# Kernel optimization log

Measured on AMD Instinct MI355X. Metric: run time of the kernel, lower is better.

The kernel has to match this reference:

```python
import jax, jax.numpy as jnp
import numpy as np

DIM = 1024
HEADS = 16
HEAD_DIM = DIM // HEADS
B, N = 4, 4096


def setup_inputs() -> dict:
    key = jax.random.key(0)
    k1, k2, k3, k4, k5 = jax.random.split(key, 5)
    scale_in = 1.0 / np.sqrt(DIM)
    return {
        "x": jax.random.normal(k1, (B, N, DIM), dtype=jnp.float32),
        # torch nn.Linear convention: weight [out, in], y = x @ W.T + b
        "w_qkv": jax.random.uniform(k2, (3 * DIM, DIM), jnp.float32, -scale_in, scale_in),
        "b_qkv": jax.random.uniform(k3, (3 * DIM,), jnp.float32, -scale_in, scale_in),
        "w_proj": jax.random.uniform(k4, (DIM, DIM), jnp.float32, -scale_in, scale_in),
        "b_proj": jax.random.uniform(k5, (DIM,), jnp.float32, -scale_in, scale_in),
    }


def reference(x, w_qkv, b_qkv, w_proj, b_proj):
    Bx, Nx, C = x.shape
    H, D = HEADS, HEAD_DIM
    qkv = (x @ w_qkv.T + b_qkv).reshape(Bx, Nx, 3, H, D)
    q, k, v = qkv[:, :, 0], qkv[:, :, 1], qkv[:, :, 2]  # each [B, N, H, D]
    # NOTE: faithful to source — heads dim was NOT moved to batch position,
    # so attention mixes across heads per token: scores [B, N, H, H].
    scores = jnp.einsum('bnhd,bngd->bnhg', q, k) / jnp.sqrt(jnp.asarray(D, x.dtype))
    attn = jax.nn.softmax(scores, axis=-1)
    out = jnp.einsum('bnhg,bngd->bnhd', attn, v).reshape(Bx, Nx, C)
    return out @ w_proj.T + b_proj
```

## Files before the change

### kernel.cpp

```cpp
#include <hip/hip_runtime.h>
#include <hip/hip_bf16.h>
#include <stdint.h>

typedef __bf16 v8bf __attribute__((ext_vector_type(8)));
typedef float  v4f  __attribute__((ext_vector_type(4)));
typedef unsigned short u16;

#define NTOK 16384
#define KDIM 1024

__device__ __forceinline__ u16 f2bf(float f) {
  uint32_t b = __builtin_bit_cast(uint32_t, f);
  b += 0x7FFFu + ((b >> 16) & 1u);
  return (u16)(b >> 16);
}

__device__ __forceinline__ void gl_lds16(const u16* g, u16* l) {
  __builtin_amdgcn_global_load_lds(
      (const __attribute__((address_space(1))) uint32_t*)g,
      (__attribute__((address_space(3))) uint32_t*)l,
      16, 0, 0);
}

__device__ __forceinline__ void bar() {
  __builtin_amdgcn_sched_barrier(0);
  __builtin_amdgcn_s_barrier();
  __builtin_amdgcn_sched_barrier(0);
}
#define LGKM0() do { asm volatile("s_waitcnt lgkmcnt(0)" ::: "memory"); \
                     __builtin_amdgcn_sched_barrier(0); } while (0)
#define VMW(n)  do { asm volatile("s_waitcnt vmcnt(" #n ")" ::: "memory"); \
                     __builtin_amdgcn_sched_barrier(0); } while (0)

__global__ void cvt_all(const float* __restrict__ x, const float* __restrict__ wq,
                        const float* __restrict__ wp, u16* __restrict__ xo,
                        u16* __restrict__ wqo, u16* __restrict__ wpo) {
  size_t id = (size_t)blockIdx.x * 256 + threadIdx.x;
  const float* src; u16* dst;
  if (id < 2097152)      { src = x  + id * 8;              dst = xo  + id * 8; }
  else if (id < 2490368) { src = wq + (id - 2097152) * 8;  dst = wqo + (id - 2097152) * 8; }
  else                   { src = wp + (id - 2490368) * 8;  dst = wpo + (id - 2490368) * 8; }
  float4 a = *(const float4*)(src);
  float4 b = *(const float4*)(src + 4);
  union { u16 u[8]; uint4 v; } pk;
  pk.u[0]=f2bf(a.x); pk.u[1]=f2bf(a.y); pk.u[2]=f2bf(a.z); pk.u[3]=f2bf(a.w);
  pk.u[4]=f2bf(b.x); pk.u[5]=f2bf(b.y); pk.u[6]=f2bf(b.z); pk.u[7]=f2bf(b.w);
  *(uint4*)(dst) = pk.v;
}

template<int NTOT, bool OUT_BF16>
__global__ __launch_bounds__(512, 1)
void gemm_bt(const u16* __restrict__ A, const u16* __restrict__ Bw,
             const float* __restrict__ bias, void* __restrict__ out) {
  constexpr int NM = NTOK / 256;
  constexpr int NN = NTOT / 256;
  constexpr int NWG = NM * NN;
  constexpr int NT = KDIM / 32;
  const int bid = blockIdx.x;
  const int swz = (bid & 7) * (NWG / 8) + (bid >> 3);
  const int bm = swz % NM, bn = swz / NM;

  extern __shared__ __align__(16) u16 smem[];
  u16* ldsA = smem;
  u16* ldsB = smem + 4 * 8192;

  const int tid = threadIdx.x, lane = tid & 63, w = tid >> 6;
  const int wr = w >> 2, wc = w & 3;

  v4f acc[8][4];
#pragma unroll
  for (int i = 0; i < 8; ++i)
#pragma unroll
    for (int j = 0; j < 4; ++j) acc[i][j] = v4f{0.f, 0.f, 0.f, 0.f};

  const u16* Ab = A  + (size_t)bm * 256 * KDIM;
  const u16* Bb = Bw + (size_t)bn * 256 * KDIM;

  const size_t soff0 = (size_t)(tid >> 2) * KDIM
      + (size_t)((((tid & 3) ^ ((tid >> 2) & 3) ^ ((tid >> 4) & 3)) & 3) * 8);
  auto stageT = [&](u16* dst, const u16* src) {
    gl_lds16(src + soff0, dst + (size_t)tid * 8);
    gl_lds16(src + soff0 + (size_t)128 * KDIM, dst + (size_t)tid * 8 + 4096);
  };

  const int cks = ((lane >> 4) ^ (lane & 3) ^ ((lane >> 2) & 3)) & 3;
  const int aoff = (wr * 128 + (lane & 15)) * 32 + cks * 8;
  const int boff = (wc * 64  + (lane & 15)) * 32 + cks * 8;

#define TILE(ST, U, DO_STAGE, VMODE) do {                                     \
  const u16* La_ = ldsA + (ST) * 8192;                                        \
  const u16* Lb_ = ldsB + (ST) * 8192;                                        \
  v8bf af[4], bf4[4];                                                         \
  _Pragma("unroll") for (int f = 0; f < 4; ++f)                               \
    af[f] = *(const v8bf*)(La_ + aoff + f * 512);                             \
  _Pragma("unroll") for (int f = 0; f < 4; ++f)                               \
    bf4[f] = *(const v8bf*)(Lb_ + boff + f * 512);                            \
  if (DO_STAGE) stageT(ldsA + (((ST) + 3) & 3) * 8192,                        \
                       Ab + (size_t)(U) * 32);                                \
  bar(); LGKM0();                                                             \
  __builtin_amdgcn_s_setprio(1);                                              \
  _Pragma("unroll") for (int qi = 0; qi < 4; ++qi)                            \
  _Pragma("unroll") for (int qj = 0; qj < 4; ++qj)                            \
    acc[qi][qj] = __builtin_amdgcn_mfma_f32_16x16x32_bf16(                    \
        af[qi], bf4[qj], acc[qi][qj], 0, 0, 0);                               \
  __builtin_amdgcn_s_setprio(0);                                              \
  bar();                                                                      \
  _Pragma("unroll") for (int f = 0; f < 4; ++f)                               \
    af[f] = *(const v8bf*)(La_ + aoff + (f + 4) * 512);                       \
  if (DO_STAGE) stageT(ldsB + (((ST) + 3) & 3) * 8192,                        \
                       Bb + (size_t)(U) * 32);                                \
  bar(); LGKM0();                                                             \
  __builtin_amdgcn_s_setprio(1);                                              \
  _Pragma("unroll") for (int qi = 0; qi < 4; ++qi)                            \
  _Pragma("unroll") for (int qj = 0; qj < 4; ++qj)                            \
    acc[4 + qi][qj] = __builtin_amdgcn_mfma_f32_16x16x32_bf16(                \
        af[qi], bf4[qj], acc[4 + qi][qj], 0, 0, 0);                           \
  __builtin_amdgcn_s_setprio(0);                                              \
  if ((VMODE) == 0) { VMW(8); }                                               \
  else if ((VMODE) == 1) { VMW(4); }                                          \
  else if ((VMODE) == 2) { VMW(0); }                                          \
  bar();                                                                      \
} while (0)

  stageT(ldsA + 0,     Ab);        stageT(ldsB + 0,     Bb);
  stageT(ldsA + 8192,  Ab + 32);   stageT(ldsB + 8192,  Bb + 32);
  stageT(ldsA + 16384, Ab + 64);   stageT(ldsB + 16384, Bb + 64);
  VMW(8);
  bar();

  for (int j = 0; j < 7; ++j) {
    const int t0 = 4 * j;
    TILE(0, t0 + 3, 1, 0);
    TILE(1, t0 + 4, 1, 0);
    TILE(2, t0 + 5, 1, 0);
    TILE(3, t0 + 6, 1, 0);
  }
  TILE(0, 31, 1, 0);
  TILE(1, 0, 0, 1);
  TILE(2, 0, 0, 2);
  TILE(3, 0, 0, 3);
#undef TILE

  const int col0 = bn * 256 + wc * 64 + (lane & 15);
  const int row0 = bm * 256 + wr * 128 + ((lane >> 4) << 2);
#pragma unroll
  for (int mf = 0; mf < 8; ++mf) {
#pragma unroll
    for (int nf = 0; nf < 4; ++nf) {
      const int gc = col0 + nf * 16;
      const float bv = bias[gc];
#pragma unroll
      for (int j = 0; j < 4; ++j) {
        const size_t idx = (size_t)(row0 + mf * 16 + j) * NTOT + gc;
        const float v = acc[mf][nf][j] + bv;
        if constexpr (OUT_BF16) ((u16*)out)[idx] = f2bf(v);
        else                    ((float*)out)[idx] = v;
      }
    }
  }
}

__global__ __launch_bounds__(256)
void attn_mix(const u16* __restrict__ qkv, u16* __restrict__ outp) {
  __shared__ __align__(16) u16 sq[4][3072];
  __shared__ float sp[4][16][16];
  const int tid = threadIdx.x, lane = tid & 63, w = tid >> 6;
  const size_t tok = (size_t)blockIdx.x * 4 + w;
  const u16* src = qkv + tok * 3072;
#pragma unroll
  for (int i = 0; i < 6; ++i) {
    int t = i * 64 + lane;
    int row = t >> 3;
    int c = (t & 7) ^ (row & 7);
    gl_lds16(src + row * 64 + c * 8, &sq[w][t * 8]);
  }
  __syncthreads();

  const int h = lane >> 2, gb = lane & 3;
  v8bf qv[8];
#pragma unroll
  for (int c = 0; c < 8; ++c)
    qv[c] = *(const v8bf*)&sq[w][h * 64 + ((c ^ (h & 7)) * 8)];

  float s[4];
#pragma unroll
  for (int g4 = 0; g4 < 4; ++g4) {
    const int g = gb * 4 + g4;
    float a = 0.f;
#pragma unroll
    for (int c = 0; c < 8; ++c) {
      v8bf kv = *(const v8bf*)&sq[w][1024 + g * 64 + ((c ^ (g & 7)) * 8)];
#pragma unroll
      for (int j = 0; j < 8; ++j) a += (float)qv[c][j] * (float)kv[j];
    }
    s[g4] = a * 0.125f;
  }
  float m = fmaxf(fmaxf(s[0], s[1]), fmaxf(s[2], s[3]));
  m = fmaxf(m, __shfl_xor(m, 1));
  m = fmaxf(m, __shfl_xor(m, 2));
  float p[4], sum = 0.f;
#pragma unroll
  for (int g4 = 0; g4 < 4; ++g4) { p[g4] = __expf(s[g4] - m); sum += p[g4]; }
  sum += __shfl_xor(sum, 1);
  sum += __shfl_xor(sum, 2);
  const float inv = 1.f / sum;
#pragma unroll
  for (int g4 = 0; g4 < 4; ++g4) sp[w][h][gb * 4 + g4] = p[g4] * inv;
  __syncthreads();

  float o[16];
#pragma unroll
  for (int j = 0; j < 16; ++j) o[j] = 0.f;
  const int db = gb;
#pragma unroll
  for (int g = 0; g < 16; ++g) {
    const float a = sp[w][h][g];
    v8bf v0 = *(const v8bf*)&sq[w][2048 + g * 64 + (((db * 2)     ^ (g & 7)) * 8)];
    v8bf v1 = *(const v8bf*)&sq[w][2048 + g * 64 + (((db * 2 + 1) ^ (g & 7)) * 8)];
#pragma unroll
    for (int j = 0; j < 8; ++j) { o[j] += a * (float)v0[j]; o[8 + j] += a * (float)v1[j]; }
  }
  union { u16 u[16]; uint4 v[2]; } ob;
#pragma unroll
  for (int j = 0; j < 16; ++j) ob.u[j] = f2bf(o[j]);
  u16* dst = outp + tok * 1024 + h * 64 + db * 16;
  *(uint4*)dst = ob.v[0];
  *((uint4*)dst + 1) = ob.v[1];
}

extern "C" void kernel_launch(void* const* d_in, const int* in_sizes, int n_in,
                              void* d_out, int out_size, void* d_ws, size_t ws_size,
                              hipStream_t stream) {
  const float* x      = (const float*)d_in[0];
  const float* w_qkv  = (const float*)d_in[1];
  const float* b_qkv  = (const float*)d_in[2];
  const float* w_proj = (const float*)d_in[3];
  const float* b_proj = (const float*)d_in[4];

  char* ws = (char*)d_ws;
  u16* x_bf    = (u16*)(ws);
  u16* wqkv_bf = (u16*)(ws + (size_t)33554432);
  u16* wp_bf   = (u16*)(ws + (size_t)39845888);
  u16* qkv_bf  = (u16*)(ws + (size_t)41943040);
  u16* at_bf   = (u16*)(ws + (size_t)142606336);

  (void)hipFuncSetAttribute((const void*)&gemm_bt<3072, true>,
                            hipFuncAttributeMaxDynamicSharedMemorySize, 131072);
  (void)hipFuncSetAttribute((const void*)&gemm_bt<1024, false>,
                            hipFuncAttributeMaxDynamicSharedMemorySize, 131072);

  cvt_all<<<dim3(10240), dim3(256), 0, stream>>>(x, w_qkv, w_proj,
                                                 x_bf, wqkv_bf, wp_bf);

  gemm_bt<3072, true ><<<dim3(768), dim3(512), 131072, stream>>>(x_bf, wqkv_bf, b_qkv, qkv_bf);
  attn_mix<<<dim3(4096), dim3(256), 0, stream>>>(qkv_bf, at_bf);
  gemm_bt<1024, false><<<dim3(256), dim3(512), 131072, stream>>>(at_bf, wp_bf, b_proj, d_out);
}
```

Baseline: 228.1 us.

## Double-buffer MFMA fragments in registers with one barrier per K-tile

After: 221.5 us. 2.9% less time.

```diff
diff --git a/kernel.cpp b/kernel.cpp
--- a/kernel.cpp
+++ b/kernel.cpp
@@ -49,7 +49,7 @@
 }
 
 template<int NTOT, bool OUT_BF16>
-__global__ __launch_bounds__(512, 1)
+__global__ __launch_bounds__(512, 2)
 void gemm_bt(const u16* __restrict__ A, const u16* __restrict__ Bw,
              const float* __restrict__ bias, void* __restrict__ out) {
   constexpr int NM = NTOK / 256;
@@ -87,39 +87,41 @@
   const int aoff = (wr * 128 + (lane & 15)) * 32 + cks * 8;
   const int boff = (wc * 64  + (lane & 15)) * 32 + cks * 8;
 
-#define TILE(ST, U, DO_STAGE, VMODE) do {                                     \
-  const u16* La_ = ldsA + (ST) * 8192;                                        \
-  const u16* Lb_ = ldsB + (ST) * 8192;                                        \
-  v8bf af[4], bf4[4];                                                         \
+  v8bf a0[4], b0[4], a1[4], b1[4];
+
+#define TILE(T, FA, FB, GA, GB, DOSTAGE, VMODE, DONEXT) do {                  \
+  const u16* La_c = ldsA + ((T) & 3) * 8192;                                  \
+  const u16* La_n = ldsA + (((T) + 1) & 3) * 8192;                            \
+  const u16* Lb_n = ldsB + (((T) + 1) & 3) * 8192;                            \
+  if ((VMODE) == 0) { VMW(4); } else if ((VMODE) == 1) { VMW(0); }            \
+  bar();                                                                      \
+  v8bf ab[4];                                                                 \
   _Pragma("unroll") for (int f = 0; f < 4; ++f)                               \
-    af[f] = *(const v8bf*)(La_ + aoff + f * 512);                             \
-  _Pragma("unroll") for (int f = 0; f < 4; ++f)                               \
-    bf4[f] = *(const v8bf*)(Lb_ + boff + f * 512);                            \
-  if (DO_STAGE) stageT(ldsA + (((ST) + 3) & 3) * 8192,                        \
-                       Ab + (size_t)(U) * 32);                                \
-  bar(); LGKM0();                                                             \
+    ab[f] = *(const v8bf*)(La_c + aoff + (f + 4) * 512);                      \
+  if (DOSTAGE) {                                                              \
+    stageT(ldsA + (((T) + 3) & 3) * 8192, Ab + (size_t)((T) + 3) * 32);       \
+    stageT(ldsB + (((T) + 3) & 3) * 8192, Bb + (size_t)((T) + 3) * 32);       \
+  }                                                                           \
   __builtin_amdgcn_s_setprio(1);                                              \
   _Pragma("unroll") for (int qi = 0; qi < 4; ++qi)                            \
   _Pragma("unroll") for (int qj = 0; qj < 4; ++qj)                            \
     acc[qi][qj] = __builtin_amdgcn_mfma_f32_16x16x32_bf16(                    \
-        af[qi], bf4[qj], acc[qi][qj], 0, 0, 0);                               \
+        FA[qi], FB[qj], acc[qi][qj], 0, 0, 0);                                \
   __builtin_amdgcn_s_setprio(0);                                              \
-  bar();                                                                      \
-  _Pragma("unroll") for (int f = 0; f < 4; ++f)                               \
-    af[f] = *(const v8bf*)(La_ + aoff + (f + 4) * 512);                       \
-  if (DO_STAGE) stageT(ldsB + (((ST) + 3) & 3) * 8192,                        \
-                       Bb + (size_t)(U) * 32);                                \
-  bar(); LGKM0();                                                             \
+  LGKM0();                                                                    \
+  if (DONEXT) {                                                               \
+    _Pragma("unroll") for (int f = 0; f < 4; ++f)                             \
+      GA[f] = *(const v8bf*)(La_n + aoff + f * 512);                          \
+    _Pragma("unroll") for (int f = 0; f < 4; ++f)                             \
+      GB[f] = *(const v8bf*)(Lb_n + boff + f * 512);                          \
+  }                                                                           \
   __builtin_amdgcn_s_setprio(1);                                              \
   _Pragma("unroll") for (int qi = 0; qi < 4; ++qi)                            \
   _Pragma("unroll") for (int qj = 0; qj < 4; ++qj)                            \
     acc[4 + qi][qj] = __builtin_amdgcn_mfma_f32_16x16x32_bf16(                \
-        af[qi], bf4[qj], acc[4 + qi][qj], 0, 0, 0);                           \
+        ab[qi], FB[qj], acc[4 + qi][qj], 0, 0, 0);                            \
   __builtin_amdgcn_s_setprio(0);                                              \
-  if ((VMODE) == 0) { VMW(8); }                                               \
-  else if ((VMODE) == 1) { VMW(4); }                                          \
-  else if ((VMODE) == 2) { VMW(0); }                                          \
-  bar();                                                                      \
+  LGKM0();                                                                    \
 } while (0)
 
   stageT(ldsA + 0,     Ab);        stageT(ldsB + 0,     Bb);
@@ -127,18 +129,21 @@
   stageT(ldsA + 16384, Ab + 64);   stageT(ldsB + 16384, Bb + 64);
   VMW(8);
   bar();
-
-  for (int j = 0; j < 7; ++j) {
-    const int t0 = 4 * j;
-    TILE(0, t0 + 3, 1, 0);
-    TILE(1, t0 + 4, 1, 0);
-    TILE(2, t0 + 5, 1, 0);
-    TILE(3, t0 + 6, 1, 0);
-  }
-  TILE(0, 31, 1, 0);
-  TILE(1, 0, 0, 1);
-  TILE(2, 0, 0, 2);
-  TILE(3, 0, 0, 3);
+#pragma unroll
+  for (int f = 0; f < 4; ++f) a0[f] = *(const v8bf*)(ldsA + aoff + f * 512);
+#pragma unroll
+  for (int f = 0; f < 4; ++f) b0[f] = *(const v8bf*)(ldsB + boff + f * 512);
+  LGKM0();
+
+  for (int j = 0; j < 14; ++j) {
+    const int t0 = 2 * j;
+    TILE(t0,     a0, b0, a1, b1, 1, 0, 1);
+    TILE(t0 + 1, a1, b1, a0, b0, 1, 0, 1);
+  }
+  TILE(28, a0, b0, a1, b1, 1, 0, 1);
+  TILE(29, a1, b1, a0, b0, 0, 0, 1);
+  TILE(30, a0, b0, a1, b1, 0, 1, 1);
+  TILE(31, a1, b1, a0, b0, 0, 2, 0);
 #undef TILE
 
   const int col0 = bn * 256 + wc * 64 + (lane & 15);
```
